# Kernel optimization log

Measured on AMD Instinct MI355X. Metric: run time of the kernel, lower is better.

## Reference

```python
import math
import jax, jax.numpy as jnp
import numpy as np

T_MIN = 0.1
T_MAX = 1.0


def _log_cond_prob(energy, text_mask, mel_mask, direction, neg):
    # energy: (B, I, J); returns (B, I, J, K) with K=J (alpha) or J-1 (beta)
    B, I, J = energy.shape
    if direction == 'alpha':
        K = J
        tri_jk = jnp.arange(J)[:, None] >= jnp.arange(K)[None, :]  # torch triu: valid if j >= k
    else:
        K = J - 1
        tri_jk = jnp.arange(J)[:, None] <= jnp.arange(K)[None, :]  # torch tril: valid if j <= k
    tm = text_mask[:, :, None, None]           # (B,I,1,1)
    mmj = mel_mask[:, None, :, None]           # (B,1,J,1)
    mmk = mel_mask[:, None, None, :K]          # (B,1,1,K)
    mask = tm & mmj & mmk                      # (B,I,J,K)
    tri = tri_jk[None, None] & mask
    mask_invalid = jnp.broadcast_to(tm & mmk, (B, I, J, K))
    text_invalid = jnp.broadcast_to(tm, (B, I, J, K))
    right_mask = mask | (~mask_invalid)
    e = jnp.broadcast_to(energy[..., None], (B, I, J, K))
    e = jnp.where((~tri) & mask_invalid, neg, e)
    e = jnp.where(~mask_invalid, -10.0, e)
    e = e - jax.nn.logsumexp(e, axis=2, keepdims=True)  # normalize over mel dim j
    e = jnp.where(~mask_invalid, neg, e)
    e = jnp.where(~right_mask, -10.0, e)
    e = jnp.where(~text_invalid, -10.0, e)
    return e


def _roll(x, shifts, axis):
    # per-batch roll of x along `axis` by shifts[b]
    return jax.vmap(lambda xb, s: jnp.roll(xb, s, axis=axis - 1))(x, shifts)


def _right_shift(x, sh_t, sh_m):
    x = _roll(x, sh_t, 1)
    x = _roll(x, sh_m, 2)
    return _roll(x, sh_m.at[1:].add(-1), 3)  # faithful to in-place shifts_mel_dim[1:] -= 1


def _left_shift(x, sh_t, sh_m):
    x = x[..., None]
    x = _roll(x, -sh_t, 1)
    x = _roll(x, -sh_m, 2)
    return x[..., 0]


def _compute_alpha(lcp_a, neg):
    # alpha[:, i, j] = lse_k(alpha[:, i-1, k] + lcp_a[:, i-1, j-1, k]) for j >= i
    B, I, J, _ = lcp_a.shape
    j_idx = jnp.arange(J + 1)
    row0 = jnp.full((B, J + 1), neg, dtype=lcp_a.dtype).at[:, 0].set(0.0)

    def step(prev, xs):  # prev = alpha[:, i-1, :J]
        lcp_i, i = xs
        new = jax.nn.logsumexp(prev[:, None, :] + lcp_i, axis=2)  # (B, J), index j-1
        row = jnp.concatenate([jnp.full((B, 1), neg, dtype=new.dtype), new], axis=1)
        row = jnp.where(j_idx[None, :] >= i, row, neg)
        return row[:, :J], row

    _, rows = jax.lax.scan(step, row0[:, :J], (jnp.swapaxes(lcp_a, 0, 1), jnp.arange(1, I + 1)))
    return jnp.concatenate([row0[:, None, :], jnp.swapaxes(rows, 0, 1)], axis=1)  # (B, I+1, J+1)


def _compute_beta(lcp_b, neg):
    # beta[:, i, j] = lse_k(beta[:, i+1, k+1] + lcp_b[:, i, j, k]) for j < J+i-I+1
    B, I, J, _ = lcp_b.shape
    j_idx = jnp.arange(J)
    last = jnp.full((B, J), neg, dtype=lcp_b.dtype).at[:, J - 1].set(0.0)

    def step(nxt, xs):
        lcp_i, i = xs
        full = jax.nn.logsumexp(nxt[:, 1:][:, None, :] + lcp_i, axis=2)  # (B, J)
        row = jnp.where(j_idx[None, :] < (J + i - I + 1), full, neg)
        return row, row

    _, rows = jax.lax.scan(step, last, (jnp.swapaxes(lcp_b[:, :I - 1], 0, 1), jnp.arange(I - 1)), reverse=True)
    return jnp.concatenate([jnp.swapaxes(rows, 0, 1), last[:, None, :]], axis=1)  # (B, I, J)


def _forward(text_embeddings, mel_embeddings, text_mask, mel_mask, noise, temperature_ratio, neg):
    B, I, Dt = text_embeddings.shape
    _, J, Dm = mel_embeddings.shape
    energy = jnp.einsum('bid,bjd->bij', text_embeddings, mel_embeddings) / math.sqrt(Dt * Dm)
    temp = T_MIN + (T_MAX - T_MIN) * temperature_ratio[0]
    energy = (energy - jnp.log(-jnp.log(noise))) / temp  # Gumbel noise + temperature
    lcp_a = _log_cond_prob(energy, text_mask, mel_mask, 'alpha', neg)
    alpha = _compute_alpha(lcp_a, neg)
    t_len = text_mask.sum(1)
    m_len = mel_mask.sum(1)
    sh_t = t_len.max() - t_len
    sh_m = m_len.max() - m_len
    lcp_b = _log_cond_prob(energy, text_mask, mel_mask, 'beta', neg)
    lcp_b = _right_shift(lcp_b, sh_t, sh_m)
    beta = _compute_beta(lcp_b, neg)
    beta = _left_shift(beta, sh_t, sh_m)
    gamma = alpha[:, 1:, 1:] + beta
    gamma_mask = text_mask[:, :, None] & mel_mask[:, None, :]
    gls_mask = jnp.broadcast_to(text_mask[:, :, None], (B, I, J)) | gamma_mask
    gamma = jnp.where(gls_mask, gamma, neg)
    gamma = gamma - jax.nn.logsumexp(gamma, axis=1, keepdims=True)  # normalize over text dim
    gamma = jnp.where(gamma_mask, gamma, neg)
    expanded = jnp.einsum('bij,bid->bjd', jnp.exp(gamma), text_embeddings)
    expanded = expanded * mel_mask[:, :, None]
    return gamma, expanded


def setup_inputs() -> dict:
    key = jax.random.key(0)
    k1, k2, k3, k4 = jax.random.split(key, 4)
    B, I, J, Dt, Dm = 1, 128, 640, 256, 256
    text_embeddings = jax.random.normal(k1, (B, I, Dt), dtype=jnp.float32)
    mel_embeddings = jax.random.normal(k2, (B, J, Dm), dtype=jnp.float32)
    text_mask = jnp.ones((B, I), dtype=bool)
    mel_mask = jnp.ones((B, J), dtype=bool)
    noise = jnp.clip(jax.random.uniform(k3, (B, I, J), dtype=jnp.float32), 1e-8, 1.0 - 1e-8)
    temperature_ratio = jax.random.uniform(k4, (1,), dtype=jnp.float32)
    return {
        'text_embeddings': text_embeddings,
        'mel_embeddings': mel_embeddings,
        'text_mask': text_mask,
        'mel_mask': mel_mask,
        'noise': noise,
        'temperature_ratio': temperature_ratio,
    }


def reference(text_embeddings, mel_embeddings, text_mask, mel_mask, noise, temperature_ratio):
    return _forward(text_embeddings, mel_embeddings, text_mask, mel_mask, noise, temperature_ratio, -jnp.inf)
```

## Files before the change

kernel.cpp:

```cpp
#include <hip/hip_runtime.h>
#include <math.h>

constexpr int TI = 128;
constexpr int TJ = 640;
constexpr int TD = 256;
constexpr int EPL = 10;

#define NEG (-1e30f)
#define LOG2E 1.44269504088896340736f
#define LN2   0.69314718055994530942f

typedef float f32x2 __attribute__((ext_vector_type(2)));
typedef float f32x4 __attribute__((ext_vector_type(4)));

__device__ __forceinline__ float rexp2(float x) { return __builtin_amdgcn_exp2f(x); }
__device__ __forceinline__ float rlog2(float x) { return __builtin_amdgcn_logf(x); }

__device__ __forceinline__ int permP(int j) {
    int l = j / 10, qq = j - l * 10;
    return (qq < 8) ? ((qq >> 2) * 256 + l * 4 + (qq & 3))
                    : (512 + l * 2 + (qq - 8));
}

struct MS { float m, s; };
__device__ __forceinline__ MS ms_combine(MS a, MS b) {
    float d = b.m - a.m;
    bool al = d <= 0.0f;
    float m = al ? a.m : b.m;
    float t = rexp2(al ? d : -d);
    float s = al ? fmaf(b.s, t, a.s) : fmaf(a.s, t, b.s);
    return {m, s};
}
__device__ __forceinline__ MS ms_push(MS run, float x) { return ms_combine(run, {x, 1.0f}); }
__device__ __forceinline__ float ms_final(MS a) {
    return (a.m < -1e29f) ? NEG : a.m + rlog2(a.s);
}

template<int CTRL, int RMASK>
__device__ __forceinline__ float dpp_f(float src, float oldv) {
    int r = __builtin_amdgcn_update_dpp(
        __float_as_int(oldv), __float_as_int(src), CTRL, RMASK, 0xF, false);
    return __int_as_float(r);
}
template<int CTRL, int RMASK>
__device__ __forceinline__ MS dpp_ms(MS v) {
    MS t;
    t.m = dpp_f<CTRL, RMASK>(v.m, NEG);
    t.s = dpp_f<CTRL, RMASK>(v.s, 0.0f);
    return t;
}
__device__ __forceinline__ MS wave_incl_scan_ms(MS v) {
    v = ms_combine(dpp_ms<0x111, 0xF>(v), v);
    v = ms_combine(dpp_ms<0x112, 0xF>(v), v);
    v = ms_combine(dpp_ms<0x114, 0xF>(v), v);
    v = ms_combine(dpp_ms<0x118, 0xF>(v), v);
    v = ms_combine(dpp_ms<0x142, 0xA>(v), v);
    v = ms_combine(dpp_ms<0x143, 0xC>(v), v);
    return v;
}
__device__ __forceinline__ MS wave_excl_from_incl_ms(MS incl) {
    return dpp_ms<0x138, 0xF>(incl);
}
__device__ __forceinline__ float wave_incl_scan_add(float v) {
    v += dpp_f<0x111, 0xF>(v, 0.0f);
    v += dpp_f<0x112, 0xF>(v, 0.0f);
    v += dpp_f<0x114, 0xF>(v, 0.0f);
    v += dpp_f<0x118, 0xF>(v, 0.0f);
    v += dpp_f<0x142, 0xA>(v, 0.0f);
    v += dpp_f<0x143, 0xC>(v, 0.0f);
    return v;
}
__device__ __forceinline__ float wave_incl_scan_max(float v) {
    v = fmaxf(v, dpp_f<0x111, 0xF>(v, NEG));
    v = fmaxf(v, dpp_f<0x112, 0xF>(v, NEG));
    v = fmaxf(v, dpp_f<0x114, 0xF>(v, NEG));
    v = fmaxf(v, dpp_f<0x118, 0xF>(v, NEG));
    v = fmaxf(v, dpp_f<0x142, 0xA>(v, NEG));
    v = fmaxf(v, dpp_f<0x143, 0xC>(v, NEG));
    return v;
}
__device__ __forceinline__ float readlane63(float v) {
    return __int_as_float(__builtin_amdgcn_readlane(__float_as_int(v), 63));
}
__device__ __forceinline__ float readlaneN(float v, int n) {
    return __int_as_float(__builtin_amdgcn_readlane(__float_as_int(v), n));
}

__global__ __launch_bounds__(256) void k_melT(
        const float* __restrict__ mel, float* __restrict__ melT) {
    __shared__ float ldsT[64][65];
    int j0 = blockIdx.x * 64, c0 = blockIdx.y * 64, tid = threadIdx.x;
    int rr = tid >> 4, c4 = tid & 15;
    #pragma unroll
    for (int p = 0; p < 4; p++) {
        int r = p * 16 + rr;
        float4 v = *(const float4*)(mel + (size_t)(j0 + r) * TD + c0 + c4 * 4);
        ldsT[c4 * 4 + 0][r] = v.x;
        ldsT[c4 * 4 + 1][r] = v.y;
        ldsT[c4 * 4 + 2][r] = v.z;
        ldsT[c4 * 4 + 3][r] = v.w;
    }
    __syncthreads();
    int jj = tid & 63, cw = tid >> 6;
    #pragma unroll
    for (int p = 0; p < 16; p++) {
        int cc = p * 4 + cw;
        melT[(size_t)(c0 + cc) * TJ + j0 + jj] = ldsT[cc][jj];
    }
}

__global__ __launch_bounds__(640) void k_energy(
        const float* __restrict__ text, const float* __restrict__ melT,
        const float* __restrict__ noise, const float* __restrict__ trat,
        float* __restrict__ energy, float* __restrict__ Ga,
        float* __restrict__ Gb, float* __restrict__ Cst) {
    __shared__ float trowm[TD], trowc[TD], trowp[TD];
    __shared__ float erowm[TJ], erowc[TJ], erowp[TJ];
    __shared__ float pcur[TJ], scur[TJ];
    __shared__ float wred[2][EPL];
    int i = blockIdx.x, tid = threadIdx.x;
    if (tid < TD) {
        trowc[tid] = text[i * TD + tid];
        trowm[tid] = (i > 0)      ? text[(i - 1) * TD + tid] : 0.0f;
        trowp[tid] = (i < TI - 1) ? text[(i + 1) * TD + tid] : 0.0f;
    }
    __syncthreads();
    float temp = 0.1f + 0.9f * trat[0];
    float sc = LOG2E / temp;
    int j = tid;
    float am = 0.0f, ac = 0.0f, ap = 0.0f;
    #pragma unroll 8
    for (int c = 0; c < TD; c++) {
        float m = melT[(size_t)c * TJ + j];
        am = fmaf(trowm[c], m, am);
        ac = fmaf(trowc[c], m, ac);
        ap = fmaf(trowp[c], m, ap);
    }
    float gm = (i > 0)      ? logf(-logf(noise[(i - 1) * TJ + j])) : 0.0f;
    float gc =                logf(-logf(noise[i * TJ + j]));
    float gp = (i < TI - 1) ? logf(-logf(noise[(i + 1) * TJ + j])) : 0.0f;
    erowm[j] = (am * (1.0f / 256.0f) - gm) * sc;
    float e2 = (ac * (1.0f / 256.0f) - gc) * sc;
    erowc[j] = e2;
    erowp[j] = (ap * (1.0f / 256.0f) - gp) * sc;
    energy[i * TJ + j] = e2;
    __syncthreads();
    if (tid < 64) {
        int l = tid;
        MS loc = {NEG, 0.0f};
        #pragma unroll
        for (int q = 0; q < EPL; q++) loc = ms_push(loc, erowc[l * EPL + q]);
        MS off = wave_excl_from_incl_ms(wave_incl_scan_ms(loc));
        MS run = off;
        #pragma unroll
        for (int q = 0; q < EPL; q++) {
            run = ms_push(run, erowc[l * EPL + q]);
            pcur[l * EPL + q] = ms_final(run);
        }
        loc = {NEG, 0.0f};
        #pragma unroll
        for (int q = 0; q < EPL; q++) loc = ms_push(loc, erowc[TJ - 1 - (l * EPL + q)]);
        off = wave_excl_from_incl_ms(wave_incl_scan_ms(loc));
        run = off;
        #pragma unroll
        for (int q = 0; q < EPL; q++) {
            int idx = TJ - 1 - (l * EPL + q);
            run = ms_push(run, erowc[idx]);
            scur[idx] = ms_final(run);
        }
    }
    __syncthreads();
    float ga, gb;
    if (i == 0) ga = (j == 0) ? -scur[0] : NEG;
    else        ga = (j == 0) ? NEG : erowm[j - 1] - scur[j];
    bool has_b = (i <= TI - 2);
    if (has_b) {
        if (i == TI - 2) gb = (j == 1) ? -pcur[TJ - 2] : NEG;
        else             gb = (j == 0) ? NEG : erowp[TJ - j] - pcur[TJ - 1 - j];
    } else gb = NEG;
    int wv = tid >> 6, l = tid & 63;
    float ma = readlane63(wave_incl_scan_max(ga));
    float mb = readlane63(wave_incl_scan_max(gb));
    if (l == 0) { wred[0][wv] = ma; wred[1][wv] = mb; }
    __syncthreads();
    float Ca = wred[0][0], Cb = wred[1][0];
    #pragma unroll
    for (int k = 1; k < EPL; k++) {
        Ca = fmaxf(Ca, wred[0][k]);
        Cb = fmaxf(Cb, wred[1][k]);
    }
    int pj = permP(j);
    Ga[i * TJ + pj] = rexp2(ga - Ca);
    if (has_b) Gb[i * TJ + pj] = rexp2(gb - Cb);
    if (tid == 0) { Cst[i] = Ca; if (has_b) Cst[TI + i] = Cb; }
}

__global__ __launch_bounds__(64, 1) void k_scan(
        const float* __restrict__ Ga, const float* __restrict__ Gb,
        const float* __restrict__ Cst,
        float* __restrict__ PpA, float* __restrict__ PpB,
        float* __restrict__ baseA, float* __restrict__ baseB) {
    constexpr int PF = 8;
    const int l = threadIdx.x;
    const bool is_alpha = (blockIdx.x == 0);
    const int nrows = is_alpha ? TI : TI - 1;
    const float* Gsrc = is_alpha ? Ga : Gb;
    float* Pdst = is_alpha ? PpA : PpB;
    float* bdst = is_alpha ? baseA : baseB;
    const int o16 = l * 16;
    const int o8  = l * 8;

#define LOADROW(S, RPTR)                                                       \
    asm volatile("global_load_dwordx4 %0, %3, %5\n\t"                          \
                 "global_load_dwordx4 %1, %3, %5 offset:1024\n\t"              \
                 "global_load_dwordx2 %2, %4, %5 offset:2048"                  \
                 : "=&v"(g4a[S]), "=&v"(g4b[S]), "=&v"(g2[S])                  \
                 : "v"(o16), "v"(o8), "s"(RPTR))

    float C0, C1;
    {
        const float* c0p = Cst + (is_alpha ? 0 : 128) + l;
        const float* c1p = c0p + 64;
        asm volatile("global_load_dword %0, %2, off\n\t"
                     "global_load_dword %1, %3, off"
                     : "=&v"(C0), "=&v"(C1) : "v"(c0p), "v"(c1p));
        asm volatile("s_waitcnt vmcnt(0)" ::: "memory");
        __builtin_amdgcn_sched_barrier(0);
    }

    f32x4 g4a[PF], g4b[PF];
    f32x2 g2[PF];
    {
        const float* r0 = Gsrc + (size_t)(is_alpha ? 0 : TI - 2) * TJ;
        const float* r1 = Gsrc + (size_t)(is_alpha ? 1 : TI - 3) * TJ;
        const float* r2 = Gsrc + (size_t)(is_alpha ? 2 : TI - 4) * TJ;
        const float* r3 = Gsrc + (size_t)(is_alpha ? 3 : TI - 5) * TJ;
        const float* r4 = Gsrc + (size_t)(is_alpha ? 4 : TI - 6) * TJ;
        const float* r5 = Gsrc + (size_t)(is_alpha ? 5 : TI - 7) * TJ;
        const float* r6 = Gsrc + (size_t)(is_alpha ? 6 : TI - 8) * TJ;
        const float* r7 = Gsrc + (size_t)(is_alpha ? 7 : TI - 9) * TJ;
        LOADROW(0, r0); LOADROW(1, r1); LOADROW(2, r2); LOADROW(3, r3);
        LOADROW(4, r4); LOADROW(5, r5); LOADROW(6, r6); LOADROW(7, r7);
    }

    float Pp[EPL];
    #pragma unroll
    for (int q = 0; q < EPL; q++) Pp[q] = 0.0f;
    float rprev = 0.0f, Lam = 0.0f;
    float bacc0 = 0.0f, bacc1 = 0.0f;

#define ROWBODY(S, T, KLIT, IS_FIRST)                                          \
    {                                                                          \
        asm volatile("s_waitcnt vmcnt(" KLIT ")" ::: "memory");                \
        __builtin_amdgcn_sched_barrier(0);                                     \
        float gv[EPL];                                                         \
        gv[0] = g4a[S][0]; gv[1] = g4a[S][1];                                  \
        gv[2] = g4a[S][2]; gv[3] = g4a[S][3];                                  \
        gv[4] = g4b[S][0]; gv[5] = g4b[S][1];                                  \
        gv[6] = g4b[S][2]; gv[7] = g4b[S][3];                                  \
        gv[8] = g2[S][0];  gv[9] = g2[S][1];                                   \
        {   \
            int tp = (T) + PF;                                                 \
            int rpi = (tp < nrows) ? tp : (nrows - 1);                         \
            int rowp = is_alpha ? rpi : (TI - 2 - rpi);                        \
            const float* gpn = Gsrc + (size_t)rowp * TJ;                       \
            LOADROW(S, gpn);                                                   \
        }                                                                      \
        float lp[EPL];                                                         \
        if (IS_FIRST) {                                                        \
            _Pragma("unroll")                                                  \
            for (int q = 0; q < EPL; q++) lp[q] = gv[q];                       \
        } else {                                                               \
            float carry = dpp_f<0x138, 0xF>(Pp[EPL - 1], 0.0f);                \
            float rp = rprev;                                                  \
            lp[0] = carry * rp * gv[0];                                        \
            _Pragma("unroll")                                                  \
            for (int q = 1; q < EPL; q++) lp[q] = Pp[q - 1] * rp * gv[q];      \
        }                                                                      \
        _Pragma("unroll")                                                      \
        for (int q = 9; q >= 1; q--) lp[q] += lp[q - 1];                       \
        _Pragma("unroll")                                                      \
        for (int q = 9; q >= 2; q--) lp[q] += lp[q - 2];                       \
        _Pragma("unroll")                                                      \
        for (int q = 9; q >= 4; q--) lp[q] += lp[q - 4];                       \
        _Pragma("unroll")                                                      \
        for (int q = 9; q >= 8; q--) lp[q] += lp[q - 8];                       \
        float incl = wave_incl_scan_add(lp[EPL - 1]);                          \
        float excl = dpp_f<0x138, 0xF>(incl, 0.0f);                            \
        _Pragma("unroll")                                                      \
        for (int q = 0; q < EPL; q++) Pp[q] = excl + lp[q];                    \
        float T_ = readlane63(incl);                                           \
        int idx2 = is_alpha ? (T) : (126 - (T));                               \
        float Cc = (idx2 < 64) ? readlaneN(C0, idx2)                           \
                               : readlaneN(C1, idx2 - 64);                     \
        float basev = Lam + Cc;                                                \
        {                \
            f32x4 p03, p47; f32x2 p89;                                         \
            p03[0] = Pp[0]; p03[1] = Pp[1]; p03[2] = Pp[2]; p03[3] = Pp[3];    \
            p47[0] = Pp[4]; p47[1] = Pp[5]; p47[2] = Pp[6]; p47[3] = Pp[7];    \
            p89[0] = Pp[8]; p89[1] = Pp[9];                                    \
            float* pp = Pdst + (size_t)(T) * TJ;                               \
            asm volatile("global_store_dwordx4 %0, %2, %5\n\t"                 \
                         "global_store_dwordx4 %0, %3, %5 offset:1024\n\t"     \
                         "global_store_dwordx2 %1, %4, %5 offset:2048"         \
                         :: "v"(o16), "v"(o8), "v"(p03), "v"(p47), "v"(p89),   \
                            "s"(pp) : "memory");                               \
        }                                                                      \
        bacc0 = ((T) == l)      ? basev : bacc0;                               \
        bacc1 = ((T) == 64 + l) ? basev : bacc1;                               \
        Lam = basev + rlog2(T_);                                               \
        rprev = (T_ > 0.0f) ? __builtin_amdgcn_rcpf(T_) : 0.0f;                \
    }

    ROWBODY(0, 0, "21", true);
    ROWBODY(1, 1, "24", false);
    ROWBODY(2, 2, "27", false);
    ROWBODY(3, 3, "30", false);
    ROWBODY(4, 4, "33", false);
    ROWBODY(5, 5, "36", false);
    ROWBODY(6, 6, "39", false);
    ROWBODY(7, 7, "42", false);

    for (int tb = PF; tb < nrows; tb += PF) {
        { int t = tb + 0; if (t < nrows) ROWBODY(0, t, "45", false); }
        { int t = tb + 1; if (t < nrows) ROWBODY(1, t, "45", false); }
        { int t = tb + 2; if (t < nrows) ROWBODY(2, t, "45", false); }
        { int t = tb + 3; if (t < nrows) ROWBODY(3, t, "45", false); }
        { int t = tb + 4; if (t < nrows) ROWBODY(4, t, "45", false); }
        { int t = tb + 5; if (t < nrows) ROWBODY(5, t, "45", false); }
        { int t = tb + 6; if (t < nrows) ROWBODY(6, t, "45", false); }
        { int t = tb + 7; if (t < nrows) ROWBODY(7, t, "45", false); }
    }

    asm volatile("s_waitcnt vmcnt(0)" ::: "memory");
    __builtin_amdgcn_sched_barrier(0);
    bdst[l] = bacc0;
    bdst[64 + l] = bacc1;
#undef ROWBODY
#undef LOADROW
}

__global__ __launch_bounds__(256) void k_gamma(
        const float* __restrict__ PpA, const float* __restrict__ PpB,
        const float* __restrict__ baseA, const float* __restrict__ baseB,
        const float* __restrict__ energy, const float* __restrict__ text,
        float* __restrict__ outg, float* __restrict__ oute) {
    __shared__ float w128[TI];
    __shared__ float redm[2], reds[2];
    int j = blockIdx.x, tid = threadIdx.x;
    int offA = permP(j);
    int offB = permP(TJ - 1 - j);
    float gg = NEG;
    if (tid < TI) {
        float ev = energy[tid * TJ + j];
        float av = ev + rlog2(PpA[tid * TJ + offA]) + baseA[tid];
        float bv;
        if (tid == TI - 1) {
            bv = (j == TJ - 1) ? 0.0f : NEG;
        } else {
            int t = TI - 2 - tid;
            bv = ev + rlog2(PpB[(size_t)t * TJ + offB]) + baseB[t];
        }
        gg = (av < -1e29f || bv < -1e29f) ? NEG : av + bv;
        MS v = {gg, 1.0f};
        #pragma unroll
        for (int off = 32; off > 0; off >>= 1) {
            float om = __shfl_xor(v.m, off, 64);
            float os = __shfl_xor(v.s, off, 64);
            v = ms_combine(v, {om, os});
        }
        if ((tid & 63) == 0) { redm[tid >> 6] = v.m; reds[tid >> 6] = v.s; }
    }
    __syncthreads();
    float lse = ms_final(ms_combine({redm[0], reds[0]}, {redm[1], reds[1]}));
    if (tid < TI) {
        bool fin = gg > -1e29f;
        outg[tid * TJ + j] = fin ? (gg - lse) * LN2 : NEG;
        w128[tid] = fin ? rexp2(gg - lse) : 0.0f;
    }
    __syncthreads();
    float acc = 0.0f;
    #pragma unroll 8
    for (int ii = 0; ii < TI; ii++) acc += w128[ii] * text[ii * TD + tid];
    oute[(size_t)j * TD + tid] = acc;
}

extern "C" void kernel_launch(void* const* d_in, const int* in_sizes, int n_in,
                              void* d_out, int out_size, void* d_ws, size_t ws_size,
                              hipStream_t stream) {
    const float* text  = (const float*)d_in[0];
    const float* mel   = (const float*)d_in[1];
    const float* noise = (const float*)d_in[4];
    const float* trat  = (const float*)d_in[5];

    float* outg = (float*)d_out;
    float* oute = outg + TI * TJ;

    float* w      = (float*)d_ws;
    float* energy = w;
    float* Ga     = w + 1 * TI * TJ;
    float* Gb     = w + 2 * TI * TJ;
    float* Cst    = Gb + (size_t)(TI - 1) * TJ;
    float* baseA  = Cst + 320;
    float* baseB  = Cst + 448;
    float* melT   = w + 3 * TI * TJ;
    float* PpA    = w + 3 * TI * TJ;
    float* PpB    = w + 4 * TI * TJ;

    k_melT  <<<dim3(TJ / 64, TD / 64), 256, 0, stream>>>(mel, melT);
    k_energy<<<TI, TJ, 0, stream>>>(text, melT, noise, trat, energy, Ga, Gb, Cst);
    k_scan  <<<2, 64, 0, stream>>>(Ga, Gb, Cst, PpA, PpB, baseA, baseB);
    k_gamma <<<TJ, 256, 0, stream>>>(PpA, PpB, baseA, baseB, energy, text, outg, oute);
}
```

Measured before the change: 123.9 us.

## Offload scan row stores to a helper wave via an LDS ring buffer

The serial scan wave now writes each prefix row into a 24-slot LDS ring and publishes progress through a shared flag. A second wave polls that flag, copies completed rows from LDS to global memory, and signals which slots are free again. The goal is to take global store traffic and vmcnt pressure off the latency-bound critical wave, and the prefetch depth also grows from 8 to 12 rows. The cost is spin-wait polling on LDS and reliance on compiler barriers rather than real fences for ordering, which could be fragile.

```diff
diff --git a/kernel.cpp b/kernel.cpp
--- a/kernel.cpp
+++ b/kernel.cpp
@@ -84,6 +84,18 @@
 }
 __device__ __forceinline__ float readlaneN(float v, int n) {
     return __int_as_float(__builtin_amdgcn_readlane(__float_as_int(v), n));
+}
+
+__device__ __forceinline__ void cbar() { asm volatile("" ::: "memory"); }
+__device__ __forceinline__ int opaque_zero(int v) {
+    int r;
+    asm("v_xor_b32 %0, %1, %1" : "=v"(r) : "v"(v));
+    return r;
+}
+__device__ __forceinline__ int pollwait(volatile int* flag, int need) {
+    int rv;
+    do { rv = *flag; } while (rv < need);
+    return rv;
 }
 
 __global__ __launch_bounds__(256) void k_melT(
@@ -195,18 +207,59 @@
     if (tid == 0) { Cst[i] = Ca; if (has_b) Cst[TI + i] = Cb; }
 }
 
-__global__ __launch_bounds__(64, 1) void k_scan(
+__global__ __launch_bounds__(128, 1) void k_scan(
         const float* __restrict__ Ga, const float* __restrict__ Gb,
         const float* __restrict__ Cst,
         float* __restrict__ PpA, float* __restrict__ PpB,
         float* __restrict__ baseA, float* __restrict__ baseB) {
-    constexpr int PF = 8;
-    const int l = threadIdx.x;
+    constexpr int PF = 12;
+    constexpr int RING = 24;
+    __shared__ float ring[RING][TJ];
+    __shared__ int prow, wfree;
+    const int l = threadIdx.x & 63;
+    const int wave = threadIdx.x >> 6;
     const bool is_alpha = (blockIdx.x == 0);
     const int nrows = is_alpha ? TI : TI - 1;
     const float* Gsrc = is_alpha ? Ga : Gb;
     float* Pdst = is_alpha ? PpA : PpB;
     float* bdst = is_alpha ? baseA : baseB;
+    if (threadIdx.x == 0) { prow = 0; wfree = 0; }
+    __syncthreads();
+
+    if (wave == 1) {
+        for (int tb = 0; tb < nrows; tb += 4) {
+            int need = (tb + 4 < nrows) ? tb + 4 : nrows;
+            int rv = pollwait((volatile int*)&prow, need);
+            cbar();
+            int tok = opaque_zero(rv);
+            f32x4 a0[4], a1[4]; f32x2 a2[4];
+            #pragma unroll
+            for (int s = 0; s < 4; s++) {
+                int t = tb + s;
+                if (t < nrows) {
+                    int sl = t % RING;
+                    const float* rp = &ring[sl][tok];
+                    a0[s] = *(const f32x4*)(rp + l * 4);
+                    a1[s] = *(const f32x4*)(rp + 256 + l * 4);
+                    a2[s] = *(const f32x2*)(rp + 512 + l * 2);
+                }
+            }
+            cbar();
+            #pragma unroll
+            for (int s = 0; s < 4; s++) {
+                int t = tb + s;
+                if (t < nrows) {
+                    float* gp = Pdst + (size_t)t * TJ;
+                    *(f32x4*)(gp + l * 4)       = a0[s];
+                    *(f32x4*)(gp + 256 + l * 4) = a1[s];
+                    *(f32x2*)(gp + 512 + l * 2) = a2[s];
+                }
+            }
+            if (l == 0) *(volatile int*)&wfree = need;
+        }
+        return;
+    }
+
     const int o16 = l * 16;
     const int o8  = l * 8;
 
@@ -230,17 +283,11 @@
 
     f32x4 g4a[PF], g4b[PF];
     f32x2 g2[PF];
-    {
-        const float* r0 = Gsrc + (size_t)(is_alpha ? 0 : TI - 2) * TJ;
-        const float* r1 = Gsrc + (size_t)(is_alpha ? 1 : TI - 3) * TJ;
-        const float* r2 = Gsrc + (size_t)(is_alpha ? 2 : TI - 4) * TJ;
-        const float* r3 = Gsrc + (size_t)(is_alpha ? 3 : TI - 5) * TJ;
-        const float* r4 = Gsrc + (size_t)(is_alpha ? 4 : TI - 6) * TJ;
-        const float* r5 = Gsrc + (size_t)(is_alpha ? 5 : TI - 7) * TJ;
-        const float* r6 = Gsrc + (size_t)(is_alpha ? 6 : TI - 8) * TJ;
-        const float* r7 = Gsrc + (size_t)(is_alpha ? 7 : TI - 9) * TJ;
-        LOADROW(0, r0); LOADROW(1, r1); LOADROW(2, r2); LOADROW(3, r3);
-        LOADROW(4, r4); LOADROW(5, r5); LOADROW(6, r6); LOADROW(7, r7);
+    #pragma unroll
+    for (int s = 0; s < PF; s++) {
+        int row = is_alpha ? s : (TI - 2 - s);
+        const float* rp = Gsrc + (size_t)row * TJ;
+        LOADROW(s, rp);
     }
 
     float Pp[EPL];
@@ -248,10 +295,11 @@
     for (int q = 0; q < EPL; q++) Pp[q] = 0.0f;
     float rprev = 0.0f, Lam = 0.0f;
     float bacc0 = 0.0f, bacc1 = 0.0f;
-
-#define ROWBODY(S, T, KLIT, IS_FIRST)                                          \
+    int seenw = 0;
+
+#define ROWBODY(S, T, IS_FIRST)                                                \
     {                                                                          \
-        asm volatile("s_waitcnt vmcnt(" KLIT ")" ::: "memory");                \
+        asm volatile("s_waitcnt vmcnt(33)" ::: "memory");                      \
         __builtin_amdgcn_sched_barrier(0);                                     \
         float gv[EPL];                                                         \
         gv[0] = g4a[S][0]; gv[1] = g4a[S][1];                                  \
@@ -294,17 +342,22 @@
         float Cc = (idx2 < 64) ? readlaneN(C0, idx2)                           \
                                : readlaneN(C1, idx2 - 64);                     \
         float basev = Lam + Cc;                                                \
-        {                \
+        {      \
+            if ((T) >= RING && seenw < (T) - RING + 1) {                       \
+                seenw = pollwait((volatile int*)&wfree, (T) - RING + 1);       \
+                cbar();                                                        \
+            }                                                                  \
+            int sl = (T) % RING;                                               \
             f32x4 p03, p47; f32x2 p89;                                         \
             p03[0] = Pp[0]; p03[1] = Pp[1]; p03[2] = Pp[2]; p03[3] = Pp[3];    \
             p47[0] = Pp[4]; p47[1] = Pp[5]; p47[2] = Pp[6]; p47[3] = Pp[7];    \
             p89[0] = Pp[8]; p89[1] = Pp[9];                                    \
-            float* pp = Pdst + (size_t)(T) * TJ;                               \
-            asm volatile("global_store_dwordx4 %0, %2, %5\n\t"                 \
-                         "global_store_dwordx4 %0, %3, %5 offset:1024\n\t"     \
-                         "global_store_dwordx2 %1, %4, %5 offset:2048"         \
-                         :: "v"(o16), "v"(o8), "v"(p03), "v"(p47), "v"(p89),   \
-                            "s"(pp) : "memory");                               \
+            float* rp_ = &ring[sl][0];                                         \
+            *(f32x4*)(rp_ + l * 4)       = p03;                                \
+            *(f32x4*)(rp_ + 256 + l * 4) = p47;                                \
+            *(f32x2*)(rp_ + 512 + l * 2) = p89;                                \
+            cbar();                                                            \
+            if (l == 0) *(volatile int*)&prow = (T) + 1;                       \
         }                                                                      \
         bacc0 = ((T) == l)      ? basev : bacc0;                               \
         bacc1 = ((T) == 64 + l) ? basev : bacc1;                               \
@@ -312,24 +365,32 @@
         rprev = (T_ > 0.0f) ? __builtin_amdgcn_rcpf(T_) : 0.0f;                \
     }
 
-    ROWBODY(0, 0, "21", true);
-    ROWBODY(1, 1, "24", false);
-    ROWBODY(2, 2, "27", false);
-    ROWBODY(3, 3, "30", false);
-    ROWBODY(4, 4, "33", false);
-    ROWBODY(5, 5, "36", false);
-    ROWBODY(6, 6, "39", false);
-    ROWBODY(7, 7, "42", false);
+    ROWBODY(0, 0, true);
+    ROWBODY(1, 1, false);
+    ROWBODY(2, 2, false);
+    ROWBODY(3, 3, false);
+    ROWBODY(4, 4, false);
+    ROWBODY(5, 5, false);
+    ROWBODY(6, 6, false);
+    ROWBODY(7, 7, false);
+    ROWBODY(8, 8, false);
+    ROWBODY(9, 9, false);
+    ROWBODY(10, 10, false);
+    ROWBODY(11, 11, false);
 
     for (int tb = PF; tb < nrows; tb += PF) {
-        { int t = tb + 0; if (t < nrows) ROWBODY(0, t, "45", false); }
-        { int t = tb + 1; if (t < nrows) ROWBODY(1, t, "45", false); }
-        { int t = tb + 2; if (t < nrows) ROWBODY(2, t, "45", false); }
-        { int t = tb + 3; if (t < nrows) ROWBODY(3, t, "45", false); }
-        { int t = tb + 4; if (t < nrows) ROWBODY(4, t, "45", false); }
-        { int t = tb + 5; if (t < nrows) ROWBODY(5, t, "45", false); }
-        { int t = tb + 6; if (t < nrows) ROWBODY(6, t, "45", false); }
-        { int t = tb + 7; if (t < nrows) ROWBODY(7, t, "45", false); }
+        { int t = tb + 0;  if (t < nrows) ROWBODY(0, t, false); }
+        { int t = tb + 1;  if (t < nrows) ROWBODY(1, t, false); }
+        { int t = tb + 2;  if (t < nrows) ROWBODY(2, t, false); }
+        { int t = tb + 3;  if (t < nrows) ROWBODY(3, t, false); }
+        { int t = tb + 4;  if (t < nrows) ROWBODY(4, t, false); }
+        { int t = tb + 5;  if (t < nrows) ROWBODY(5, t, false); }
+        { int t = tb + 6;  if (t < nrows) ROWBODY(6, t, false); }
+        { int t = tb + 7;  if (t < nrows) ROWBODY(7, t, false); }
+        { int t = tb + 8;  if (t < nrows) ROWBODY(8, t, false); }
+        { int t = tb + 9;  if (t < nrows) ROWBODY(9, t, false); }
+        { int t = tb + 10; if (t < nrows) ROWBODY(10, t, false); }
+        { int t = tb + 11; if (t < nrows) ROWBODY(11, t, false); }
     }
 
     asm volatile("s_waitcnt vmcnt(0)" ::: "memory");
@@ -409,6 +470,6 @@
 
     k_melT  <<<dim3(TJ / 64, TD / 64), 256, 0, stream>>>(mel, melT);
     k_energy<<<TI, TJ, 0, stream>>>(text, melT, noise, trat, energy, Ga, Gb, Cst);
-    k_scan  <<<2, 64, 0, stream>>>(Ga, Gb, Cst, PpA, PpB, baseA, baseB);
+    k_scan  <<<2, 128, 0, stream>>>(Ga, Gb, Cst, PpA, PpB, baseA, baseB);
     k_gamma <<<TJ, 256, 0, stream>>>(PpA, PpB, baseA, baseB, energy, text, outg, oute);
 }
```

Measured after the change: 146.1 us. 17.9% more time.
